# Optimization experiments

Hardware: AMD Instinct MI355X
Metric: run time of the kernel (lower is better)

The kernel has to match this reference:

```python
import jax, jax.numpy as jnp
from jax import lax
import numpy as np
import math

B, N, M, SIG, HID, NFEAT, OUT, H = 256, 512, 16, 256, 256, 3, 10, 256
ALPHA, BETA = 1.0, 0.5


def setup_inputs() -> dict:
    key = jax.random.key(0)
    ks = jax.random.split(key, 12)
    s_g = 1.0 / math.sqrt(HID)
    s_f = 1.0 / math.sqrt(SIG)
    return {
        "x": jax.random.normal(ks[0], (B, 1, H, H), jnp.float32),
        "unif": jax.random.uniform(ks[1], (B, N), jnp.float32),
        "z": jax.random.normal(ks[2], (B, N, 2), jnp.float32),
        "m_g_params": jax.random.normal(ks[3], (1, 6 * M), jnp.float32),
        "gc1_w": jax.random.uniform(ks[4], (NFEAT, HID), jnp.float32, -s_g, s_g),
        "gc1_b": jax.random.uniform(ks[5], (HID,), jnp.float32, -s_g, s_g),
        "gc2_w": jax.random.uniform(ks[6], (HID, HID), jnp.float32, -s_g, s_g),
        "gc2_b": jax.random.uniform(ks[7], (HID,), jnp.float32, -s_g, s_g),
        "collapser1": 0.1 * jax.random.normal(ks[8], (SIG, N), jnp.float32),
        "collapser2": 0.1 * jax.random.normal(ks[9], (SIG, N), jnp.float32),
        "fcf_w": jax.random.uniform(ks[10], (OUT, SIG), jnp.float32, -s_f, s_f),
        "fcf_b": jax.random.uniform(ks[11], (OUT,), jnp.float32, -s_f, s_f),
    }


def _mixture_fields(m_g_params):
    # torch: split [num_sample, 6M] into M chunks of 6, stack -> [M, N, 6],
    # split along last dim, then .view(N, M) in C-order on the [M, N] field.
    raw = m_g_params.reshape(M, 6)  # [M, 6]
    return [jnp.broadcast_to(raw[:, j][:, None], (M, N)).reshape(N, M) for j in range(6)]


def reference(x, unif, z, m_g_params, gc1_w, gc1_b, gc2_w, gc2_b,
              collapser1, collapser2, fcf_w, fcf_b):
    pi_f, mux_f, muy_f, sx_f, sy_f, rho_f = _mixture_fields(m_g_params)
    pi = jax.nn.softmax(pi_f, axis=-1)            # [N, M]
    # categorical sampling via CDF inversion, vectorized over batch
    cdf = jnp.cumsum(pi, axis=-1)                 # [N, M]
    idx = jnp.argmax(unif[:, :, None] < cdf[None], axis=-1)  # [B, N]
    row = jnp.arange(N)[None, :]
    gat = lambda f: f[row, idx]                   # [B, N]
    mux, muy = gat(mux_f), gat(muy_f)
    sx, sy = jnp.exp(gat(sx_f)), jnp.exp(gat(sy_f))
    rho = jnp.tanh(gat(rho_f))
    # reparameterized bivariate-normal sample via Cholesky (lower)
    z1, z2 = z[..., 0], z[..., 1]
    xs = mux + sx * z1
    ys = muy + sy * (rho * z1 + jnp.sqrt(1.0 - rho * rho) * z2)
    # torch MVN.sample() is no_grad -> detach samples
    xs_c, ys_c = lax.stop_gradient(xs), lax.stop_gradient(ys)
    dx, dy = xs_c - mux, ys_c - muy
    omr2 = 1.0 - rho * rho
    quad = (dx * dx / (sx * sx) - 2.0 * rho * dx * dy / (sx * sy) + dy * dy / (sy * sy)) / omr2
    logprob = (-jnp.log(2.0 * jnp.pi) - jnp.log(sx * sy)
               - 0.5 * jnp.log(omr2) - 0.5 * quad)  # [B, N]
    full_log_prob = logprob.sum(axis=-1)           # [B]
    loc = jnp.tanh(jnp.stack([xs_c, ys_c], axis=-1))  # [B, N, 2]
    # adjacency: inverse shifted pairwise squared distance
    diff = loc[:, :, None, :] - loc[:, None, :, :]  # [B, N, N, 2]
    adj = 1.0 / (ALPHA + BETA * jnp.sum(diff * diff, axis=-1))  # [B, N, N]
    # pixel gather: denormalize (trunc toward zero, like torch .long())
    pix = jnp.trunc(0.5 * (loc + 1.0) * H - 0.1).astype(jnp.int32)
    pix = jnp.clip(pix, 0, H - 1)
    bidx = jnp.arange(B)[:, None]
    pv = x[bidx, :, pix[..., 0], pix[..., 1]]      # [B, N, 1]
    feat = jnp.concatenate([pv, loc], axis=-1)     # [B, N, 3]
    # GCN (eval mode: no dropout)
    s1 = jax.nn.relu(jnp.einsum('bnm,bmh->bnh', adj, feat @ gc1_w) + gc1_b)
    s2 = jax.nn.relu(jnp.einsum('bnm,bmh->bnh', adj, s1 @ gc2_w) + gc2_b)
    # nn.Softmax() (no dim) on 3D input resolves to dim=0 in torch
    g1 = jax.nn.softmax(jnp.einsum('sn,bnh->bsh', collapser1, s1), axis=0)
    g2 = jax.nn.softmax(jnp.einsum('sn,bnh->bsh', collapser2, s2), axis=0)
    sig = (g1 + g2).sum(axis=2)                    # [B, SIG]
    out = jax.nn.softmax(sig @ fcf_w.T + fcf_b, axis=-1)  # [B, OUT]
    return out, full_log_prob
```

## Files before the change

kernel.cpp:

```cpp
#include <hip/hip_runtime.h>
#include <hip/hip_bf16.h>
#include <math.h>

#define Bx   256
#define Nx   512
#define SIGx 256
#define HIDx 256
#define OUTx 10
#define Hx   256

typedef __attribute__((ext_vector_type(4))) float f32x4;
typedef long fp8x8;
typedef unsigned char uchar;

#define WAITVM(N) asm volatile("s_waitcnt vmcnt(" #N ")" ::: "memory")
#define MEMFENCE() asm volatile("" ::: "memory")

__device__ inline uchar f2fp8(float v) {
    int r = __builtin_amdgcn_cvt_pk_fp8_f32(v, 0.0f, 0, false);
    return (uchar)(r & 0xff);
}
__device__ inline uint pk4fp8(float a0, float a1, float a2, float a3) {
    int r = __builtin_amdgcn_cvt_pk_fp8_f32(a0, a1, 0, false);
    r = __builtin_amdgcn_cvt_pk_fp8_f32(a2, a3, r, true);
    return (uint)r;
}

__device__ inline void gload_lds16(const uchar* g, uchar* l) {
    __builtin_amdgcn_global_load_lds(
        (const __attribute__((address_space(1))) uint*)g,
        (__attribute__((address_space(3))) uint*)l, 16, 0, 0);
}
__device__ inline const uchar* laddr(const uchar* base, int row, int kb) {
    int ps = (kb >> 4) ^ ((row >> 1) & 3) ^ ((row >> 4) & 3);
    return base + row*64 + ps*16 + (kb & 15);
}

__global__ __launch_bounds__(512) void kA_sample(
    const float* __restrict__ x, const float* __restrict__ z,
    const float* __restrict__ mg, float* __restrict__ feat,
    float* __restrict__ flp)
{
    int b = blockIdx.x;
    int n = threadIdx.x;
    int g = n >> 5;
    float mux = mg[g*6+1];
    float muy = mg[g*6+2];
    float sxv = expf(mg[g*6+3]);
    float syv = expf(mg[g*6+4]);
    float rho = tanhf(mg[g*6+5]);
    float z1 = z[((size_t)b*Nx + n)*2 + 0];
    float z2 = z[((size_t)b*Nx + n)*2 + 1];
    float omr2 = 1.0f - rho*rho;
    float xs = mux + sxv*z1;
    float ys = muy + syv*(rho*z1 + sqrtf(omr2)*z2);
    float dx = xs - mux, dy = ys - muy;
    float quad = (dx*dx/(sxv*sxv) - 2.0f*rho*dx*dy/(sxv*syv) + dy*dy/(syv*syv)) / omr2;
    float logprob = -1.8378770664093453f - logf(sxv*syv) - 0.5f*logf(omr2) - 0.5f*quad;
    float lx = tanhf(xs), ly = tanhf(ys);
    int px = (int)truncf(0.5f*(lx+1.0f)*(float)Hx - 0.1f);
    int py = (int)truncf(0.5f*(ly+1.0f)*(float)Hx - 0.1f);
    px = px < 0 ? 0 : (px > Hx-1 ? Hx-1 : px);
    py = py < 0 ? 0 : (py > Hx-1 ? Hx-1 : py);
    float pv = x[(size_t)b*Hx*Hx + (size_t)px*Hx + py];
    size_t fo = ((size_t)b*Nx + n)*3;
    feat[fo+0] = pv; feat[fo+1] = lx; feat[fo+2] = ly;

    __shared__ float red[512];
    red[n] = logprob;
    __syncthreads();
    for (int st = 256; st > 0; st >>= 1) {
        if (n < st) red[n] += red[n+st];
        __syncthreads();
    }
    if (n == 0) flp[b] = red[0];
}

__global__ __launch_bounds__(256) void kPrep(
    const float* __restrict__ c1, const float* __restrict__ c2,
    const float* __restrict__ w2,
    uchar* __restrict__ c1q, uchar* __restrict__ c2q, uchar* __restrict__ w2tq)
{
    int idx = blockIdx.x*256 + threadIdx.x;
    if (idx < SIGx*Nx) {
        c1q[idx] = f2fp8(16.0f * c1[idx]);
        c2q[idx] = f2fp8(16.0f * c2[idx]);
    }
    if (idx < HIDx*HIDx) {
        int i = idx >> 8, j = idx & 255;
        w2tq[idx] = f2fp8(16.0f * w2[j*HIDx + i]);
    }
}

__global__ __launch_bounds__(512) void kFuse1(
    const float* __restrict__ featL, const float* __restrict__ w1,
    const float* __restrict__ b1,
    uchar* __restrict__ adjAll, uchar* __restrict__ s1tAll)
{
    int b = blockIdx.x;
    const float* fb = featL + (size_t)b*Nx*3;
    uchar* adj = adjAll + (size_t)b*Nx*Nx;
    uchar* s1t = s1tAll + (size_t)b*HIDx*Nx;

    __shared__ float fpv[Nx], flx[Nx], fly[Nx], fH[Nx];
    __shared__ float w1s[3*HIDx], b1s[HIDx];
    __shared__ float Gp[4][3][Nx];

    int t = threadIdx.x;
    {
        float pv = fb[t*3+0], lx = fb[t*3+1], ly = fb[t*3+2];
        fpv[t] = pv; flx[t] = lx; fly[t] = ly;
        fH[t] = fmaf(0.5f*lx, lx, fmaf(0.5f*ly, ly, 1.0f));
    }
    for (int i = t; i < 3*HIDx; i += 512) w1s[i] = w1[i];
    if (t < HIDx) b1s[t] = b1[t];
    __syncthreads();

    int tq = t & 127;
    int mc = t >> 7;
    int n4 = tq*4;

    float xn[4], yn[4], cn[4];
    #pragma unroll
    for (int e = 0; e < 4; ++e) {
        xn[e] = flx[n4+e]; yn[e] = fly[n4+e];
        cn[e] = fmaf(0.5f*xn[e], xn[e], 0.5f*yn[e]*yn[e]);
    }
    float G0[4] = {}, G1[4] = {}, G2[4] = {};

    int m0 = mc*128;
    #pragma unroll 4
    for (int mm = 0; mm < 128; ++mm) {
        int m = m0 + mm;
        float hx = fH[m], fx = flx[m], fy = fly[m];
        float a[4];
        #pragma unroll
        for (int e = 0; e < 4; ++e) {
            float s = fmaf(-yn[e], fy, fmaf(-xn[e], fx, hx + cn[e]));
            a[e] = __builtin_amdgcn_rcpf(s);
            G0[e] = fmaf(a[e], fpv[m], G0[e]);
            G1[e] = fmaf(a[e], fx, G1[e]);
            G2[e] = fmaf(a[e], fy, G2[e]);
        }
        *(uint*)(adj + (size_t)m*Nx + n4) = pk4fp8(a[0], a[1], a[2], a[3]);
    }

    *(f32x4*)&Gp[mc][0][n4] = (f32x4){G0[0],G0[1],G0[2],G0[3]};
    *(f32x4*)&Gp[mc][1][n4] = (f32x4){G1[0],G1[1],G1[2],G1[3]};
    *(f32x4*)&Gp[mc][2][n4] = (f32x4){G2[0],G2[1],G2[2],G2[3]};
    __syncthreads();

    f32x4 T0 = {}, T1 = {}, T2 = {};
    #pragma unroll
    for (int j = 0; j < 4; ++j) {
        T0 += *(const f32x4*)&Gp[j][0][n4];
        T1 += *(const f32x4*)&Gp[j][1][n4];
        T2 += *(const f32x4*)&Gp[j][2][n4];
    }

    int hc = mc;
    #pragma unroll 4
    for (int hh = 0; hh < 64; ++hh) {
        int h = hc*64 + hh;
        float w0 = w1s[h], wA = w1s[HIDx+h], wB = w1s[2*HIDx+h], bb = b1s[h];
        float v0 = fminf(fmaxf(fmaf(T0.x,w0, fmaf(T1.x,wA, fmaf(T2.x,wB, bb))), 0.0f), 448.0f);
        float v1 = fminf(fmaxf(fmaf(T0.y,w0, fmaf(T1.y,wA, fmaf(T2.y,wB, bb))), 0.0f), 448.0f);
        float v2 = fminf(fmaxf(fmaf(T0.z,w0, fmaf(T1.z,wA, fmaf(T2.z,wB, bb))), 0.0f), 448.0f);
        float v3 = fminf(fmaxf(fmaf(T0.w,w0, fmaf(T1.w,wA, fmaf(T2.w,wB, bb))), 0.0f), 448.0f);
        *(uint*)(s1t + (size_t)h*Nx + n4) = pk4fp8(v0, v1, v2, v3);
    }
}

__global__ __launch_bounds__(512, 4) void kGemmAdj8(
    const uchar* __restrict__ Aall, const uchar* __restrict__ adjAll,
    const float* __restrict__ bias, uchar* __restrict__ outAll)
{
    int b    = blockIdx.x;
    int tile = blockIdx.y;
    int rt = tile >> 2;
    int ct = tile & 3;
    const uchar* A = Aall + (size_t)b*HIDx*Nx;
    const uchar* Badj = adjAll + (size_t)b*Nx*Nx;
    uchar* outp = outAll + (size_t)b*HIDx*Nx;

    __shared__ __align__(16) uchar Als[3][128*64];
    __shared__ __align__(16) uchar Bls[3][128*64];
    int t = threadIdx.x;
    int lane = t & 63, wave = t >> 6;
    int wr = wave >> 2, wc = wave & 3;
    int q = lane >> 4, c16 = lane & 15;
    int r0 = rt*128, n0 = ct*128;
    int srow = wave*16 + (lane >> 2);
    int pu   = lane & 3;
    int sl   = pu ^ ((srow>>1)&3) ^ ((srow>>4)&3);
    f32x4 acc[4][2] = {};

    auto stage = [&](int buf, int kkv) {
        gload_lds16(A + (size_t)(r0+srow)*Nx + kkv + sl*16, Als[buf] + wave*1024);
        gload_lds16(Badj + (size_t)(n0+srow)*Nx + kkv + sl*16, Bls[buf] + wave*1024);
    };

    const int nt = Nx/64;
    stage(0, 0);
    stage(1, 64);
    for (int i = 0; i < nt; ++i) {
        if (i < nt-2) { stage((i+2)%3, (i+2)*64); WAITVM(4); }
        else if (i == nt-2) WAITVM(2);
        else WAITVM(0);
        __builtin_amdgcn_s_barrier();
        MEMFENCE();
        const uchar* Ac = Als[i%3];
        const uchar* Bc = Bls[i%3];
        #pragma unroll
        for (int ks = 0; ks < 64; ks += 32) {
            fp8x8 af[4], bfr[2];
            #pragma unroll
            for (int i2 = 0; i2 < 4; ++i2)
                af[i2] = *(const fp8x8*)laddr(Ac, wr*64 + i2*16 + c16, ks + q*8);
            #pragma unroll
            for (int j = 0; j < 2; ++j)
                bfr[j] = *(const fp8x8*)laddr(Bc, wc*32 + j*16 + c16, ks + q*8);
            #pragma unroll
            for (int i2 = 0; i2 < 4; ++i2)
                #pragma unroll
                for (int j = 0; j < 2; ++j)
                    acc[i2][j] = __builtin_amdgcn_mfma_f32_16x16x32_fp8_fp8(af[i2], bfr[j], acc[i2][j], 0, 0, 0);
        }
        MEMFENCE();
        __builtin_amdgcn_s_barrier();
        MEMFENCE();
    }
    #pragma unroll
    for (int i = 0; i < 4; ++i) {
        int rowb = r0 + wr*64 + i*16 + q*4;
        #pragma unroll
        for (int j = 0; j < 2; ++j) {
            int col = n0 + wc*32 + j*16 + c16;
            #pragma unroll
            for (int r = 0; r < 4; ++r) {
                float v = fmaxf(acc[i][j][r] + bias[rowb + r], 0.0f) * 0.25f;
                outp[(size_t)(rowb + r)*Nx + col] = f2fp8(fminf(v, 448.0f));
            }
        }
    }
}

__global__ __launch_bounds__(512, 4) void kGstd8(
    const uchar* __restrict__ Ash, const uchar* __restrict__ Ball,
    uchar* __restrict__ outAll, float oscale)
{
    int b    = blockIdx.x;
    int tile = blockIdx.y;
    int rt = tile >> 1;
    int ct = tile & 1;
    const uchar* B = Ball + (size_t)b*HIDx*Nx;
    uchar* outp = outAll + (size_t)b*HIDx*256;

    __shared__ __align__(16) uchar Als[3][128*64];
    __shared__ __align__(16) uchar Bls[3][128*64];
    int t = threadIdx.x;
    int lane = t & 63, wave = t >> 6;
    int wr = wave >> 2, wc = wave & 3;
    int q = lane >> 4, c16 = lane & 15;
    int r0 = rt*128, n0 = ct*128;
    int srow = wave*16 + (lane >> 2);
    int pu   = lane & 3;
    int sl   = pu ^ ((srow>>1)&3) ^ ((srow>>4)&3);
    f32x4 acc[4][2] = {};

    auto stage = [&](int buf, int kkv) {
        gload_lds16(Ash + (size_t)(r0+srow)*Nx + kkv + sl*16, Als[buf] + wave*1024);
        gload_lds16(B + (size_t)(n0+srow)*Nx + kkv + sl*16, Bls[buf] + wave*1024);
    };

    const int nt = Nx/64;
    stage(0, 0);
    stage(1, 64);
    for (int i = 0; i < nt; ++i) {
        if (i < nt-2) { stage((i+2)%3, (i+2)*64); WAITVM(4); }
        else if (i == nt-2) WAITVM(2);
        else WAITVM(0);
        __builtin_amdgcn_s_barrier();
        MEMFENCE();
        const uchar* Ac = Als[i%3];
        const uchar* Bc = Bls[i%3];
        #pragma unroll
        for (int ks = 0; ks < 64; ks += 32) {
            fp8x8 af[4], bfr[2];
            #pragma unroll
            for (int i2 = 0; i2 < 4; ++i2)
                af[i2] = *(const fp8x8*)laddr(Ac, wr*64 + i2*16 + c16, ks + q*8);
            #pragma unroll
            for (int j = 0; j < 2; ++j)
                bfr[j] = *(const fp8x8*)laddr(Bc, wc*32 + j*16 + c16, ks + q*8);
            #pragma unroll
            for (int i2 = 0; i2 < 4; ++i2)
                #pragma unroll
                for (int j = 0; j < 2; ++j)
                    acc[i2][j] = __builtin_amdgcn_mfma_f32_16x16x32_fp8_fp8(af[i2], bfr[j], acc[i2][j], 0, 0, 0);
        }
        MEMFENCE();
        __builtin_amdgcn_s_barrier();
        MEMFENCE();
    }
    #pragma unroll
    for (int i = 0; i < 4; ++i) {
        int rowb = r0 + wr*64 + i*16 + q*4;
        #pragma unroll
        for (int j = 0; j < 2; ++j) {
            int col = n0 + wc*32 + j*16 + c16;
            #pragma unroll
            for (int r = 0; r < 4; ++r) {
                float v = acc[i][j][r] * oscale;
                v = fminf(fmaxf(v, -448.0f), 448.0f);
                outp[(size_t)(rowb + r)*256 + col] = f2fp8(v);
            }
        }
    }
}

template<int K, int NC, bool TRB>
__global__ __launch_bounds__(256) void kGstdP(
    const uchar* __restrict__ Ash, const uchar* __restrict__ Ball,
    uchar* __restrict__ outAll, float oscale)
{
    constexpr int CT = NC / 128;
    int b    = blockIdx.x;
    int tile = blockIdx.y;
    int rt = tile / CT;
    int ct = tile % CT;
    const uchar* B = Ball + (size_t)b*HIDx*Nx;
    uchar* outp = outAll + (size_t)b*HIDx*NC;

    __shared__ __align__(16) uchar Als[2][128*64];
    __shared__ __align__(16) uchar Bls[2][128*64];
    int t = threadIdx.x;
    int lane = t & 63, wave = t >> 6;
    int wr = wave >> 1, wc = wave & 1;
    int q = lane >> 4, c16 = lane & 15;
    int r0 = rt*128, n0 = ct*128;
    int lrow = lane >> 2;
    int pu   = lane & 3;
    int pi  = t & 31;
    int nc8 = t >> 5;
    f32x4 acc[4][4] = {};

    auto stageAsync = [&](int buf, int kkv) {
        #pragma unroll
        for (int r = 0; r < 2; ++r) {
            int chunk = wave*2 + r;
            int row = chunk*16 + lrow;
            int sl = pu ^ ((row>>1)&3) ^ ((row>>4)&3);
            gload_lds16(Ash + (size_t)(r0+row)*K + kkv + sl*16, Als[buf] + chunk*1024);
            if (!TRB)
                gload_lds16(B + (size_t)(n0+row)*K + kkv + sl*16, Bls[buf] + chunk*1024);
        }
    };
    auto mfmaStep = [&](int buf) {
        const uchar* Ac = Als[buf];
        const uchar* Bc = Bls[buf];
        #pragma unroll
        for (int ks = 0; ks < 64; ks += 32) {
            fp8x8 af[4], bfr[4];
            #pragma unroll
            for (int i = 0; i < 4; ++i)
                af[i] = *(const fp8x8*)laddr(Ac, wr*64 + i*16 + c16, ks + q*8);
            #pragma unroll
            for (int j = 0; j < 4; ++j)
                bfr[j] = *(const fp8x8*)laddr(Bc, wc*64 + j*16 + c16, ks + q*8);
            #pragma unroll
            for (int i = 0; i < 4; ++i)
                #pragma unroll
                for (int j = 0; j < 4; ++j)
                    acc[i][j] = __builtin_amdgcn_mfma_f32_16x16x32_fp8_fp8(af[i], bfr[j], acc[i][j], 0, 0, 0);
        }
    };

    auto loadBT = [&](int kkv, float4& v0, float4& v1) {
        int hk = kkv + 2*pi;
        const uchar* g0 = B + (size_t)hk*NC + n0 + nc8*16;
        v0 = *(const float4*)g0;
        v1 = *(const float4*)(g0 + NC);
    };
    auto writeBT = [&](int buf, const float4& v0, const float4& v1) {
        const uchar* pa = (const uchar*)&v0;
        const uchar* qa = (const uchar*)&v1;
        int kb = 2*pi;
        int s  = kb >> 4;
        #pragma unroll
        for (int e = 0; e < 16; ++e) {
            int row = nc8*16 + e;
            int ps = s ^ ((row>>1)&3) ^ ((row>>4)&3);
            *(ushort*)(Bls[buf] + row*64 + ps*16 + (kb & 15)) =
                (ushort)pa[e] | ((ushort)qa[e] << 8);
        }
    };
    float4 bv0, bv1;
    stageAsync(0, 0);
    if (TRB) { loadBT(0, bv0, bv1); writeBT(0, bv0, bv1); }
    __syncthreads();
    int cur = 0;
    for (int kk = 0; kk < K; kk += 64) {
        int nxt = cur ^ 1;
        bool more = (kk + 64) < K;
        if (more) {
            stageAsync(nxt, kk + 64);
            if (TRB) loadBT(kk + 64, bv0, bv1);
        }
        mfmaStep(cur);
        if (more && TRB) writeBT(nxt, bv0, bv1);
        __syncthreads();
        cur = nxt;
    }
    #pragma unroll
    for (int i = 0; i < 4; ++i) {
        int rowb = r0 + wr*64 + i*16 + q*4;
        #pragma unroll
        for (int j = 0; j < 4; ++j) {
            int col = n0 + wc*64 + j*16 + c16;
            #pragma unroll
            for (int r = 0; r < 4; ++r) {
                float v = acc[i][j][r] * oscale;
                v = fminf(fmaxf(v, -448.0f), 448.0f);
                outp[(size_t)(rowb + r)*NC + col] = f2fp8(v);
            }
        }
    }
}

__global__ __launch_bounds__(512) void kF1q(
    const uchar* __restrict__ t1, const uchar* __restrict__ t2,
    float* __restrict__ m1, float* __restrict__ rd1,
    float* __restrict__ m2, float* __restrict__ rd2)
{
    int s = blockIdx.x;
    int t = threadIdx.x;
    int hq = t & 63;
    int bq = t >> 6;
    const size_t str = (size_t)SIGx*HIDx;
    size_t base = (size_t)(bq*32)*str + (size_t)s*HIDx + hq*4;

    float mv1[4], dv1[4], mv2[4], dv2[4];
    #pragma unroll
    for (int e = 0; e < 4; ++e) { mv1[e]=-3.0e38f; dv1[e]=0.0f; mv2[e]=-3.0e38f; dv2[e]=0.0f; }

    for (int i = 0; i < 32; ++i) {
        uint u1 = *(const uint*)(t1 + base + (size_t)i*str);
        uint u2 = *(const uint*)(t2 + base + (size_t)i*str);
        float v1[4], v2[4];
        v1[0] = __builtin_amdgcn_cvt_f32_fp8(u1, 0);
        v1[1] = __builtin_amdgcn_cvt_f32_fp8(u1, 1);
        v1[2] = __builtin_amdgcn_cvt_f32_fp8(u1, 2);
        v1[3] = __builtin_amdgcn_cvt_f32_fp8(u1, 3);
        v2[0] = __builtin_amdgcn_cvt_f32_fp8(u2, 0);
        v2[1] = __builtin_amdgcn_cvt_f32_fp8(u2, 1);
        v2[2] = __builtin_amdgcn_cvt_f32_fp8(u2, 2);
        v2[3] = __builtin_amdgcn_cvt_f32_fp8(u2, 3);
        #pragma unroll
        for (int e = 0; e < 4; ++e) {
            float mn;
            mn = fmaxf(mv1[e], v1[e]);
            dv1[e] = dv1[e]*__expf(mv1[e]-mn) + __expf(v1[e]-mn); mv1[e] = mn;
            mn = fmaxf(mv2[e], v2[e]);
            dv2[e] = dv2[e]*__expf(mv2[e]-mn) + __expf(v2[e]-mn); mv2[e] = mn;
        }
    }

    __shared__ float pm1[8][256], pd1[8][256], pm2[8][256], pd2[8][256];
    #pragma unroll
    for (int e = 0; e < 4; ++e) {
        pm1[bq][hq*4+e] = mv1[e]; pd1[bq][hq*4+e] = dv1[e];
        pm2[bq][hq*4+e] = mv2[e]; pd2[bq][hq*4+e] = dv2[e];
    }
    __syncthreads();

    if (t < 256) {
        int h = t;
        float m = -3.0e38f, d = 0.0f;
        #pragma unroll
        for (int j = 0; j < 8; ++j) {
            float mm = pm1[j][h], dd = pd1[j][h];
            float mn = fmaxf(m, mm);
            d = d*__expf(m-mn) + dd*__expf(mm-mn);
            m = mn;
        }
        size_t o = (size_t)s*HIDx + h;
        m1[o] = m; rd1[o] = 1.0f/d;
    } else {
        int h = t - 256;
        float m = -3.0e38f, d = 0.0f;
        #pragma unroll
        for (int j = 0; j < 8; ++j) {
            float mm = pm2[j][h], dd = pd2[j][h];
            float mn = fmaxf(m, mm);
            d = d*__expf(m-mn) + dd*__expf(mm-mn);
            m = mn;
        }
        size_t o = (size_t)s*HIDx + h;
        m2[o] = m; rd2[o] = 1.0f/d;
    }
}

__global__ __launch_bounds__(256) void kF2q(
    const uchar* __restrict__ t1, const uchar* __restrict__ t2,
    const float* __restrict__ m1, const float* __restrict__ rd1,
    const float* __restrict__ m2, const float* __restrict__ rd2,
    float* __restrict__ sig)
{
    int b = blockIdx.y;
    int sq = threadIdx.x >> 6;
    int s = blockIdx.x*4 + sq;
    int hq = threadIdx.x & 63;
    size_t sh = (size_t)s*HIDx + hq*4;
    size_t tb = ((size_t)b*SIGx + s)*HIDx + hq*4;
    uint u1 = *(const uint*)(t1 + tb);
    uint u2 = *(const uint*)(t2 + tb);
    f32x4 a1 = *(const f32x4*)&m1[sh];
    f32x4 r1 = *(const f32x4*)&rd1[sh];
    f32x4 a2 = *(const f32x4*)&m2[sh];
    f32x4 r2 = *(const f32x4*)&rd2[sh];
    float v = 0.0f;
    v += __expf(__builtin_amdgcn_cvt_f32_fp8(u1,0) - a1.x) * r1.x;
    v += __expf(__builtin_amdgcn_cvt_f32_fp8(u1,1) - a1.y) * r1.y;
    v += __expf(__builtin_amdgcn_cvt_f32_fp8(u1,2) - a1.z) * r1.z;
    v += __expf(__builtin_amdgcn_cvt_f32_fp8(u1,3) - a1.w) * r1.w;
    v += __expf(__builtin_amdgcn_cvt_f32_fp8(u2,0) - a2.x) * r2.x;
    v += __expf(__builtin_amdgcn_cvt_f32_fp8(u2,1) - a2.y) * r2.y;
    v += __expf(__builtin_amdgcn_cvt_f32_fp8(u2,2) - a2.z) * r2.z;
    v += __expf(__builtin_amdgcn_cvt_f32_fp8(u2,3) - a2.w) * r2.w;

    __shared__ float red[256];
    red[threadIdx.x] = v;
    __syncthreads();
    for (int st = 32; st > 0; st >>= 1) {
        if (hq < st) red[threadIdx.x] += red[threadIdx.x + st];
        __syncthreads();
    }
    if (hq == 0) sig[(size_t)b*SIGx + s] = red[sq*64];
}

__global__ __launch_bounds__(256) void kG_out(
    const float* __restrict__ sig, const float* __restrict__ fw,
    const float* __restrict__ fb, float* __restrict__ out)
{
    int b = blockIdx.x;
    int tid = threadIdx.x;
    __shared__ float red[256];
    __shared__ float logits[OUTx];
    float sv = sig[(size_t)b*SIGx + tid];
    for (int o = 0; o < OUTx; ++o) {
        red[tid] = sv * fw[o*SIGx + tid];
        __syncthreads();
        for (int st = 128; st > 0; st >>= 1) {
            if (tid < st) red[tid] += red[tid+st];
            __syncthreads();
        }
        if (tid == 0) logits[o] = red[0] + fb[o];
        __syncthreads();
    }
    if (tid == 0) {
        float mx = logits[0];
        for (int o = 1; o < OUTx; ++o) mx = fmaxf(mx, logits[o]);
        float dd = 0.0f; float e[OUTx];
        for (int o = 0; o < OUTx; ++o) { e[o] = expf(logits[o]-mx); dd += e[o]; }
        float inv = 1.0f/dd;
        for (int o = 0; o < OUTx; ++o) out[(size_t)b*OUTx + o] = e[o]*inv;
    }
}

static inline size_t alignup(size_t b) { return (b + 255) & ~(size_t)255; }

extern "C" void kernel_launch(void* const* d_in, const int* in_sizes, int n_in,
                              void* d_out, int out_size, void* d_ws, size_t ws_size,
                              hipStream_t stream)
{
    const float* x   = (const float*)d_in[0];
    const float* z   = (const float*)d_in[2];
    const float* mg  = (const float*)d_in[3];
    const float* w1  = (const float*)d_in[4];
    const float* b1  = (const float*)d_in[5];
    const float* w2  = (const float*)d_in[6];
    const float* b2  = (const float*)d_in[7];
    const float* c1  = (const float*)d_in[8];
    const float* c2  = (const float*)d_in[9];
    const float* fw  = (const float*)d_in[10];
    const float* fbv = (const float*)d_in[11];
    float* out = (float*)d_out;
    float* flp = out + (size_t)Bx*OUTx;
    (void)in_sizes; (void)n_in; (void)out_size;

    char* ws = (char*)d_ws;
    size_t off = 0;
    auto alloc = [&](size_t bytes) -> char* {
        char* p = ws + off; off += alignup(bytes); return p;
    };
    float*  feat = (float*)alloc((size_t)Bx*Nx*3*4);
    uchar*  c1q  = (uchar*)alloc((size_t)SIGx*Nx);
    uchar*  c2q  = (uchar*)alloc((size_t)SIGx*Nx);
    uchar*  w2tq = (uchar*)alloc((size_t)HIDx*HIDx);
    uchar*  t1   = (uchar*)alloc((size_t)Bx*SIGx*HIDx);
    uchar*  t2   = (uchar*)alloc((size_t)Bx*SIGx*HIDx);
    float*  m1   = (float*)alloc((size_t)SIGx*HIDx*4);
    float*  d1   = (float*)alloc((size_t)SIGx*HIDx*4);
    float*  m2   = (float*)alloc((size_t)SIGx*HIDx*4);
    float*  d2   = (float*)alloc((size_t)SIGx*HIDx*4);
    float*  sig  = (float*)alloc((size_t)Bx*SIGx*4);
    size_t fixed = off;

    int BC = 1;
    for (int c = Bx; c >= 1; c >>= 1) {
        size_t need = fixed + alignup((size_t)c*Nx*Nx)
                            + 2*alignup((size_t)c*HIDx*Nx);
        if (need <= ws_size) { BC = c; break; }
    }
    uchar* Padj = (uchar*)alloc((size_t)BC*Nx*Nx);
    uchar* P1   = (uchar*)alloc((size_t)BC*HIDx*Nx);
    uchar* P2   = (uchar*)alloc((size_t)BC*HIDx*Nx);

    hipLaunchKernelGGL(kA_sample, dim3(Bx), dim3(Nx), 0, stream, x, z, mg, feat, flp);
    hipLaunchKernelGGL(kPrep, dim3(512), dim3(256), 0, stream, c1, c2, w2, c1q, c2q, w2tq);

    const int nch = Bx / BC;
    for (int c = 0; c < nch; ++c) {
        int b0 = c * BC;
        const float* featL = feat + (size_t)b0*Nx*3;
        uchar* t1L = t1 + (size_t)b0*SIGx*HIDx;
        uchar* t2L = t2 + (size_t)b0*SIGx*HIDx;
        hipLaunchKernelGGL(kFuse1, dim3(BC), dim3(512), 0, stream,
                           featL, w1, b1, Padj, P2);
        hipLaunchKernelGGL(kGstd8, dim3(BC, 4), dim3(512), 0, stream,
                           c1q, P2, t1L, 0.0625f);
        hipLaunchKernelGGL((kGstdP<256,512,true>), dim3(BC, 8), dim3(256), 0, stream,
                           w2tq, P2, P1, 0.0625f);
        hipLaunchKernelGGL(kGemmAdj8, dim3(BC, 8), dim3(512), 0, stream, P1, Padj, b2, P2);
        hipLaunchKernelGGL(kGstd8, dim3(BC, 4), dim3(512), 0, stream,
                           c2q, P2, t2L, 0.25f);
    }

    hipLaunchKernelGGL(kF1q, dim3(SIGx), dim3(512), 0, stream,
                       t1, t2, m1, d1, m2, d2);
    hipLaunchKernelGGL(kF2q, dim3(SIGx/4, Bx), dim3(256), 0, stream,
                       t1, t2, m1, d1, m2, d2, sig);
    hipLaunchKernelGGL(kG_out, dim3(Bx), dim3(256), 0, stream, sig, fw, fbv, out);
}
```

Before: 289.2 us.

## Switch fp8 GEMMs to double buffering and widen transposed GEMM to 512 threads

Drops kGemmAdj8 and kGstd8 from a three-stage to a two-stage LDS pipeline, halving shared memory per block so more blocks can be resident per CU. Replaces the templated 256-thread transposed-B GEMM with a 512-thread kernel that computes the same tile with 8 waves, each holding a 64x32 accumulator, and uses narrower 8-byte B loads for the transposing LDS write. The trade is less global-load latency hiding per block in exchange for more occupancy and more waves in the transposed GEMM.

```diff
diff --git a/kernel.cpp b/kernel.cpp
--- a/kernel.cpp
+++ b/kernel.cpp
@@ -10,6 +10,7 @@
 #define Hx   256
 
 typedef __attribute__((ext_vector_type(4))) float f32x4;
+typedef __attribute__((ext_vector_type(2))) uint uint2v;
 typedef long fp8x8;
 typedef unsigned char uchar;
 
@@ -183,8 +184,8 @@
     const uchar* Badj = adjAll + (size_t)b*Nx*Nx;
     uchar* outp = outAll + (size_t)b*HIDx*Nx;
 
-    __shared__ __align__(16) uchar Als[3][128*64];
-    __shared__ __align__(16) uchar Bls[3][128*64];
+    __shared__ __align__(16) uchar Als[2][128*64];
+    __shared__ __align__(16) uchar Bls[2][128*64];
     int t = threadIdx.x;
     int lane = t & 63, wave = t >> 6;
     int wr = wave >> 2, wc = wave & 3;
@@ -202,15 +203,13 @@
 
     const int nt = Nx/64;
     stage(0, 0);
-    stage(1, 64);
     for (int i = 0; i < nt; ++i) {
-        if (i < nt-2) { stage((i+2)%3, (i+2)*64); WAITVM(4); }
-        else if (i == nt-2) WAITVM(2);
+        if (i < nt-1) { stage((i+1)&1, (i+1)*64); WAITVM(2); }
         else WAITVM(0);
         __builtin_amdgcn_s_barrier();
         MEMFENCE();
-        const uchar* Ac = Als[i%3];
-        const uchar* Bc = Bls[i%3];
+        const uchar* Ac = Als[i&1];
+        const uchar* Bc = Bls[i&1];
         #pragma unroll
         for (int ks = 0; ks < 64; ks += 32) {
             fp8x8 af[4], bfr[2];
@@ -256,8 +255,8 @@
     const uchar* B = Ball + (size_t)b*HIDx*Nx;
     uchar* outp = outAll + (size_t)b*HIDx*256;
 
-    __shared__ __align__(16) uchar Als[3][128*64];
-    __shared__ __align__(16) uchar Bls[3][128*64];
+    __shared__ __align__(16) uchar Als[2][128*64];
+    __shared__ __align__(16) uchar Bls[2][128*64];
     int t = threadIdx.x;
     int lane = t & 63, wave = t >> 6;
     int wr = wave >> 2, wc = wave & 3;
@@ -275,15 +274,13 @@
 
     const int nt = Nx/64;
     stage(0, 0);
-    stage(1, 64);
     for (int i = 0; i < nt; ++i) {
-        if (i < nt-2) { stage((i+2)%3, (i+2)*64); WAITVM(4); }
-        else if (i == nt-2) WAITVM(2);
+        if (i < nt-1) { stage((i+1)&1, (i+1)*64); WAITVM(2); }
         else WAITVM(0);
         __builtin_amdgcn_s_barrier();
         MEMFENCE();
-        const uchar* Ac = Als[i%3];
-        const uchar* Bc = Bls[i%3];
+        const uchar* Ac = Als[i&1];
+        const uchar* Bc = Bls[i&1];
         #pragma unroll
         for (int ks = 0; ks < 64; ks += 32) {
             fp8x8 af[4], bfr[2];
@@ -319,16 +316,15 @@
     }
 }
 
-template<int K, int NC, bool TRB>
-__global__ __launch_bounds__(256) void kGstdP(
+__global__ __launch_bounds__(512, 4) void kGstdT8(
     const uchar* __restrict__ Ash, const uchar* __restrict__ Ball,
     uchar* __restrict__ outAll, float oscale)
 {
-    constexpr int CT = NC / 128;
+    const int K = 256, NC = 512;
     int b    = blockIdx.x;
     int tile = blockIdx.y;
-    int rt = tile / CT;
-    int ct = tile % CT;
+    int rt = tile >> 2;
+    int ct = tile & 3;
     const uchar* B = Ball + (size_t)b*HIDx*Nx;
     uchar* outp = outAll + (size_t)b*HIDx*NC;
 
@@ -336,24 +332,38 @@
     __shared__ __align__(16) uchar Bls[2][128*64];
     int t = threadIdx.x;
     int lane = t & 63, wave = t >> 6;
-    int wr = wave >> 1, wc = wave & 1;
+    int wr = wave >> 2, wc = wave & 3;
     int q = lane >> 4, c16 = lane & 15;
     int r0 = rt*128, n0 = ct*128;
-    int lrow = lane >> 2;
+    int srow = wave*16 + (lane >> 2);
     int pu   = lane & 3;
+    int sl   = pu ^ ((srow>>1)&3) ^ ((srow>>4)&3);
     int pi  = t & 31;
-    int nc8 = t >> 5;
-    f32x4 acc[4][4] = {};
-
-    auto stageAsync = [&](int buf, int kkv) {
-        #pragma unroll
-        for (int r = 0; r < 2; ++r) {
-            int chunk = wave*2 + r;
-            int row = chunk*16 + lrow;
-            int sl = pu ^ ((row>>1)&3) ^ ((row>>4)&3);
-            gload_lds16(Ash + (size_t)(r0+row)*K + kkv + sl*16, Als[buf] + chunk*1024);
-            if (!TRB)
-                gload_lds16(B + (size_t)(n0+row)*K + kkv + sl*16, Bls[buf] + chunk*1024);
+    int g   = t >> 5;
+    int nc8 = g & 7;
+    int ch  = g >> 3;
+    f32x4 acc[4][2] = {};
+
+    auto stageA = [&](int buf, int kkv) {
+        gload_lds16(Ash + (size_t)(r0+srow)*K + kkv + sl*16, Als[buf] + wave*1024);
+    };
+    auto loadBT = [&](int kkv, uint2v& v0, uint2v& v1) {
+        int hk = kkv + 2*pi;
+        const uchar* g0 = B + (size_t)hk*NC + n0 + nc8*16 + ch*8;
+        v0 = *(const uint2v*)g0;
+        v1 = *(const uint2v*)(g0 + NC);
+    };
+    auto writeBT = [&](int buf, const uint2v& v0, const uint2v& v1) {
+        const uchar* pa = (const uchar*)&v0;
+        const uchar* qa = (const uchar*)&v1;
+        int kb = 2*pi;
+        int s  = kb >> 4;
+        #pragma unroll
+        for (int e = 0; e < 8; ++e) {
+            int row = nc8*16 + ch*8 + e;
+            int ps = s ^ ((row>>1)&3) ^ ((row>>4)&3);
+            *(ushort*)(Bls[buf] + row*64 + ps*16 + (kb & 15)) =
+                (ushort)pa[e] | ((ushort)qa[e] << 8);
         }
     };
     auto mfmaStep = [&](int buf) {
@@ -361,63 +371,42 @@
         const uchar* Bc = Bls[buf];
         #pragma unroll
         for (int ks = 0; ks < 64; ks += 32) {
-            fp8x8 af[4], bfr[4];
+            fp8x8 af[4], bfr[2];
             #pragma unroll
             for (int i = 0; i < 4; ++i)
                 af[i] = *(const fp8x8*)laddr(Ac, wr*64 + i*16 + c16, ks + q*8);
             #pragma unroll
-            for (int j = 0; j < 4; ++j)
-                bfr[j] = *(const fp8x8*)laddr(Bc, wc*64 + j*16 + c16, ks + q*8);
+            for (int j = 0; j < 2; ++j)
+                bfr[j] = *(const fp8x8*)laddr(Bc, wc*32 + j*16 + c16, ks + q*8);
             #pragma unroll
             for (int i = 0; i < 4; ++i)
                 #pragma unroll
-                for (int j = 0; j < 4; ++j)
+                for (int j = 0; j < 2; ++j)
                     acc[i][j] = __builtin_amdgcn_mfma_f32_16x16x32_fp8_fp8(af[i], bfr[j], acc[i][j], 0, 0, 0);
         }
     };
 
-    auto loadBT = [&](int kkv, float4& v0, float4& v1) {
-        int hk = kkv + 2*pi;
-        const uchar* g0 = B + (size_t)hk*NC + n0 + nc8*16;
-        v0 = *(const float4*)g0;
-        v1 = *(const float4*)(g0 + NC);
-    };
-    auto writeBT = [&](int buf, const float4& v0, const float4& v1) {
-        const uchar* pa = (const uchar*)&v0;
-        const uchar* qa = (const uchar*)&v1;
-        int kb = 2*pi;
-        int s  = kb >> 4;
-        #pragma unroll
-        for (int e = 0; e < 16; ++e) {
-            int row = nc8*16 + e;
-            int ps = s ^ ((row>>1)&3) ^ ((row>>4)&3);
-            *(ushort*)(Bls[buf] + row*64 + ps*16 + (kb & 15)) =
-                (ushort)pa[e] | ((ushort)qa[e] << 8);
-        }
-    };
-    float4 bv0, bv1;
-    stageAsync(0, 0);
-    if (TRB) { loadBT(0, bv0, bv1); writeBT(0, bv0, bv1); }
+    uint2v bv0, bv1;
+    stageA(0, 0);
+    loadBT(0, bv0, bv1); writeBT(0, bv0, bv1);
     __syncthreads();
-    int cur = 0;
     for (int kk = 0; kk < K; kk += 64) {
-        int nxt = cur ^ 1;
+        int cur = (kk >> 6) & 1, nxt = cur ^ 1;
         bool more = (kk + 64) < K;
         if (more) {
-            stageAsync(nxt, kk + 64);
-            if (TRB) loadBT(kk + 64, bv0, bv1);
+            stageA(nxt, kk + 64);
+            loadBT(kk + 64, bv0, bv1);
         }
         mfmaStep(cur);
-        if (more && TRB) writeBT(nxt, bv0, bv1);
+        if (more) writeBT(nxt, bv0, bv1);
         __syncthreads();
-        cur = nxt;
     }
     #pragma unroll
     for (int i = 0; i < 4; ++i) {
         int rowb = r0 + wr*64 + i*16 + q*4;
         #pragma unroll
-        for (int j = 0; j < 4; ++j) {
-            int col = n0 + wc*64 + j*16 + c16;
+        for (int j = 0; j < 2; ++j) {
+            int col = n0 + wc*32 + j*16 + c16;
             #pragma unroll
             for (int r = 0; r < 4; ++r) {
                 float v = acc[i][j][r] * oscale;
@@ -630,7 +619,7 @@
                            featL, w1, b1, Padj, P2);
         hipLaunchKernelGGL(kGstd8, dim3(BC, 4), dim3(512), 0, stream,
                            c1q, P2, t1L, 0.0625f);
-        hipLaunchKernelGGL((kGstdP<256,512,true>), dim3(BC, 8), dim3(256), 0, stream,
+        hipLaunchKernelGGL(kGstdT8, dim3(BC, 8), dim3(512), 0, stream,
                            w2tq, P2, P1, 0.0625f);
         hipLaunchKernelGGL(kGemmAdj8, dim3(BC, 8), dim3(512), 0, stream, P1, Padj, b2, P2);
         hipLaunchKernelGGL(kGstd8, dim3(BC, 4), dim3(512), 0, stream,
```

Result: no change. 288.4 us (-0.3%).
